# Kernel optimization log

Hardware: AMD Instinct MI355X
Metric: run time of the kernel (lower is better)

## Reference

```python
import jax, jax.numpy as jnp
import numpy as np

B, S, D, H, HD = 4096, 50, 32, 4, 8
SCALE = 1.0 / (8 ** 0.5)


def setup_inputs() -> dict:
    key = jax.random.key(0)
    ks = jax.random.split(key, 12)
    inp = {
        'Q': jax.random.normal(ks[0], (B, S, D), dtype=jnp.float32),
        'K': jax.random.normal(ks[1], (B, S, D), dtype=jnp.float32),
        'V': jax.random.normal(ks[2], (B, S, D), dtype=jnp.float32),
        'mask': jax.random.randint(ks[3], (B, 1, S, S), 0, 2).astype(jnp.bool_),
        # Linear weights (stored as [in, out]; equivalent math to torch's x @ W.T + b)
        'WQ': jax.random.normal(ks[4], (D, D), dtype=jnp.float32) * 0.1,
        'bQ': jnp.zeros((D,), dtype=jnp.float32),
        'WK': jax.random.normal(ks[5], (D, D), dtype=jnp.float32) * 0.1,
        'bK': jnp.zeros((D,), dtype=jnp.float32),
        'WV': jax.random.normal(ks[6], (D, D), dtype=jnp.float32) * 0.1,
        'bV': jnp.zeros((D,), dtype=jnp.float32),
        'WO': jax.random.normal(ks[7], (D, D), dtype=jnp.float32) * 0.1,
        'bO': jnp.zeros((D,), dtype=jnp.float32),
    }
    return inp


def reference(Q, K, V, mask, WQ, bQ, WK, bK, WV, bV, WO, bO):
    qSrc = Q
    # fcQ/fcK/fcV are (faithfully) applied twice, as in the original forward
    q = (Q @ WQ + bQ) @ WQ + bQ
    k = (K @ WK + bK) @ WK + bK
    v = (V @ WV + bV) @ WV + bV
    # split heads: [B, S, D] -> [B, H, S, HD]
    q = q.reshape(B, S, H, HD).transpose(0, 2, 1, 3)
    k = k.reshape(B, S, H, HD).transpose(0, 2, 1, 3)
    v = v.reshape(B, S, H, HD).transpose(0, 2, 1, 3)
    score = jnp.einsum('bhqd,bhkd->bhqk', q, k) * SCALE
    score = jnp.where(mask, -jnp.inf, score)
    attn = jax.nn.softmax(score, axis=-1)
    ctx = jnp.einsum('bhqk,bhkd->bhqd', attn, v)
    ctx = ctx.transpose(0, 2, 1, 3).reshape(B, S, D)
    out = ctx @ WO + bO  # dropout is identity in eval mode
    return qSrc + out
```

## Files before the change

### kernel.cpp

```cpp
#include <hip/hip_runtime.h>

#define NB 4096
constexpr float kQscale = 0.35355339059327378f * 1.4426950408889634f;

constexpr int ST = 40;
constexpr int SP = 72;
constexpr int SV = 72;
constexpr int OFF_W  = 0;
constexpr int OFF_A  = 5120;
constexpr int OFF_C  = 7680;
constexpr int OFF_B  = 10240;
constexpr int OFF_V2 = 12800;
constexpr int SH_LEN = 15104;

typedef __attribute__((ext_vector_type(8))) short bf16x8;
typedef __attribute__((ext_vector_type(4))) float f32x4;

__device__ __forceinline__ unsigned cvt2(float lo, float hi) {
  unsigned u;
  asm("v_cvt_pk_bf16_f32 %0, %1, %2" : "=v"(u) : "v"(lo), "v"(hi));
  return u;
}
__device__ __forceinline__ float fexp2(float x) {
  float r;
  asm("v_exp_f32 %0, %1" : "=v"(r) : "v"(x));
  return r;
}

__global__ __launch_bounds__(256) void mha(
    const float* __restrict__ Qg, const float* __restrict__ Kg,
    const float* __restrict__ Vg, const void* __restrict__ maskg,
    const float* __restrict__ WQg, const float* __restrict__ bQg,
    const float* __restrict__ WKg, const float* __restrict__ bKg,
    const float* __restrict__ WVg, const float* __restrict__ bVg,
    const float* __restrict__ WOg, const float* __restrict__ bOg,
    float* __restrict__ outg)
{
  __shared__ __align__(16) short SH[SH_LEN];
  __shared__ __align__(16) float sBias[128];
  __shared__ unsigned sRaw[80];
  __shared__ unsigned sMask[128];

  const int t = threadIdx.x;
  const int b = blockIdx.x;
  const int lane = t & 63;
  const int wv = t >> 6;
  const int c = lane & 15, g = lane >> 4;
  const int myrow = wv*16 + c;

  auto stage_tile = [&](const float* __restrict__ src, int dstOff) {
    #pragma unroll
    for (int it = 0; it < 2; ++it) {
      const int idx = t + it*256;
      if (idx < 400) {
        const float4 x = ((const float4*)src)[idx];
        const int s = idx >> 3, qd = idx & 7;
        *(uint2*)&SH[dstOff + s*ST + qd*4] = make_uint2(cvt2(x.x, x.y), cvt2(x.z, x.w));
      }
    }
  };

  auto projX = [&](int xOff, int wm, int biasOff, int yOff, float scale) {
    const bf16x8 xb = *(const bf16x8*)&SH[xOff + myrow*ST + g*8];
    #pragma unroll
    for (int Ni = 0; Ni < 2; ++Ni) {
      const bf16x8 wa = *(const bf16x8*)&SH[OFF_W + wm*1280 + (Ni*16 + c)*ST + g*8];
      const float4 bv = *(const float4*)&sBias[biasOff + Ni*16 + g*4];
      f32x4 acc = {bv.x, bv.y, bv.z, bv.w};
      acc = __builtin_amdgcn_mfma_f32_16x16x32_bf16(wa, xb, acc, 0, 0, 0);
      *(uint2*)&SH[yOff + myrow*ST + Ni*16 + g*4] =
          make_uint2(cvt2(acc[0]*scale, acc[1]*scale), cvt2(acc[2]*scale, acc[3]*scale));
    }
  };

  stage_tile(Kg + b*1600, OFF_A);
  stage_tile(Qg + b*1600, OFF_C);
  stage_tile(Vg + b*1600, OFF_B);
  #pragma unroll
  for (int m = 0; m < 4; ++m) {
    const float* Wp = (m == 0) ? WQg : (m == 1) ? WKg : (m == 2) ? WVg : WOg;
    const float4 x = ((const float4*)Wp)[t];
    const int k = t >> 3, d0 = (t & 7)*4;
    const unsigned u0 = cvt2(x.x, x.y), u1 = cvt2(x.z, x.w);
    SH[OFF_W + m*1280 + (d0+0)*ST + k] = (short)(u0 & 0xFFFF);
    SH[OFF_W + m*1280 + (d0+1)*ST + k] = (short)(u0 >> 16);
    SH[OFF_W + m*1280 + (d0+2)*ST + k] = (short)(u1 & 0xFFFF);
    SH[OFF_W + m*1280 + (d0+3)*ST + k] = (short)(u1 >> 16);
  }
  if      (t < 32)  sBias[t] = bQg[t];
  else if (t < 64)  sBias[t] = bKg[t-32];
  else if (t < 96)  sBias[t] = bVg[t-64];
  else if (t < 128) sBias[t] = bOg[t-96];
  {
    const unsigned w64 = ((const unsigned*)maskg)[lane];
    const bool byteMask = (__ballot(w64 > 1u) != 0ull);
    const int mbase = b * 2500;
    for (int ch = wv*10; ch < wv*10 + 10; ++ch) {
      const int idx = ch*64 + lane;
      unsigned val = 0;
      if (idx < 2500) {
        val = byteMask ? (unsigned)((const unsigned char*)maskg)[mbase + idx]
                       : (unsigned)((const unsigned*)maskg)[mbase + idx];
      }
      const unsigned long long m = __ballot(val != 0u);
      if (lane == 0) {
        sRaw[ch*2]     = (unsigned)m;
        sRaw[ch*2 + 1] = (unsigned)(m >> 32);
      }
    }
  }
  __syncthreads();

  if (t < 100) {
    const int i = t >> 1, half = t & 1;
    const int bitpos = 50*i + half*32;
    const int a = bitpos >> 5, sh = bitpos & 31;
    unsigned w = sRaw[a] >> sh;
    if (sh) w |= sRaw[a+1] << (32 - sh);
    sMask[t] = w;
  }
  projX(OFF_A, 1, 32, OFF_A, 1.f);
  projX(OFF_A, 1, 32, OFF_A, 1.f);
  projX(OFF_B, 2, 64, OFF_B, 1.f);
  {
    const bf16x8 a = *(const bf16x8*)&SH[OFF_B + myrow*ST + g*8];
    #pragma unroll
    for (int Nj = 0; Nj < 2; ++Nj) {
      const bf16x8 bb = *(const bf16x8*)&SH[OFF_W + 2*1280 + (Nj*16 + c)*ST + g*8];
      const float bv = sBias[64 + Nj*16 + c];
      f32x4 acc = {bv, bv, bv, bv};
      acc = __builtin_amdgcn_mfma_f32_16x16x32_bf16(a, bb, acc, 0, 0, 0);
      const int j0 = wv*16 + g*4;
      const float v0 = (j0+0 < 50) ? acc[0] : 0.f;
      const float v1 = (j0+1 < 50) ? acc[1] : 0.f;
      const float v2 = (j0+2 < 50) ? acc[2] : 0.f;
      const float v3 = (j0+3 < 50) ? acc[3] : 0.f;
      *(uint2*)&SH[OFF_V2 + (Nj*16 + c)*SV + j0] = make_uint2(cvt2(v0,v1), cvt2(v2,v3));
    }
  }
  projX(OFF_C, 0, 0, OFF_C, 1.f);
  projX(OFF_C, 0, 0, OFF_C, kQscale);
  __syncthreads();

  f32x4 s[4][4];
  {
    const bf16x8 qb = *(const bf16x8*)&SH[OFF_C + myrow*ST + g*8];
    const bf16x8 zf = {0,0,0,0,0,0,0,0};
    #pragma unroll
    for (int Ni = 0; Ni < 4; ++Ni) {
      const bf16x8 kf = *(const bf16x8*)&SH[OFF_A + (Ni*16 + c)*ST + g*8];
      #pragma unroll
      for (int h = 0; h < 4; ++h) {
        const bf16x8 af = (g == h) ? kf : zf;
        f32x4 z = {0.f, 0.f, 0.f, 0.f};
        s[h][Ni] = __builtin_amdgcn_mfma_f32_16x16x32_bf16(af, qb, z, 0, 0, 0);
      }
    }
  }
  __syncthreads();

  const unsigned m0 = (myrow < 50) ? sMask[myrow*2]     : 0xFFFFFFFFu;
  const unsigned m1 = (myrow < 50) ? sMask[myrow*2 + 1] : 0xFFFFFFFFu;
  bool keep[4][4];
  #pragma unroll
  for (int Ni = 0; Ni < 4; ++Ni) {
    const unsigned w = (Ni < 2) ? m0 : m1;
    #pragma unroll
    for (int r = 0; r < 4; ++r) {
      const int key = Ni*16 + g*4 + r;
      keep[Ni][r] = (key < 50) && (((w >> (key & 31)) & 1u) == 0u);
    }
  }

  short* SPp = &SH[OFF_A];
  #pragma unroll
  for (int h = 0; h < 4; ++h) {
    float ps[4][4];
    float rs = 0.f;
    #pragma unroll
    for (int Ni = 0; Ni < 4; ++Ni) {
      #pragma unroll
      for (int r = 0; r < 4; ++r) {
        const float e = fexp2(s[h][Ni][r]);
        const float p = keep[Ni][r] ? e : 0.f;
        ps[Ni][r] = p;
        rs += p;
      }
    }
    rs += __shfl_xor(rs, 16);
    rs += __shfl_xor(rs, 32);
    const float ri = __builtin_amdgcn_rcpf(rs);
    #pragma unroll
    for (int Ni = 0; Ni < 4; ++Ni)
      *(uint2*)&SPp[myrow*SP + Ni*16 + g*4] =
          make_uint2(cvt2(ps[Ni][0], ps[Ni][1]), cvt2(ps[Ni][2], ps[Ni][3]));
    f32x4 cac = {0.f, 0.f, 0.f, 0.f};
    #pragma unroll
    for (int ks = 0; ks < 2; ++ks) {
      const bf16x8 vf = *(const bf16x8*)&SH[OFF_V2 + (h*8 + (c & 7))*SV + ks*32 + g*8];
      const bf16x8 pf = *(const bf16x8*)&SPp[myrow*SP + ks*32 + g*8];
      cac = __builtin_amdgcn_mfma_f32_16x16x32_bf16(vf, pf, cac, 0, 0, 0);
    }
    if (g < 2)
      *(uint2*)&SH[OFF_B + myrow*ST + h*8 + g*4] =
          make_uint2(cvt2(cac[0]*ri, cac[1]*ri), cvt2(cac[2]*ri, cac[3]*ri));
  }

  {
    const bf16x8 af = *(const bf16x8*)&SH[OFF_B + myrow*ST + g*8];
    #pragma unroll
    for (int Nj = 0; Nj < 2; ++Nj) {
      const bf16x8 bbf = *(const bf16x8*)&SH[OFF_W + 3*1280 + (Nj*16 + c)*ST + g*8];
      const float bv = sBias[96 + Nj*16 + c];
      f32x4 o = {bv, bv, bv, bv};
      o = __builtin_amdgcn_mfma_f32_16x16x32_bf16(af, bbf, o, 0, 0, 0);
      #pragma unroll
      for (int r = 0; r < 4; ++r) {
        const int row = wv*16 + g*4 + r;
        if (row < 50) {
          const int gi = b*1600 + row*32 + Nj*16 + c;
          outg[gi] = o[r] + Qg[gi];
        }
      }
    }
  }
}

extern "C" void kernel_launch(void* const* d_in, const int* in_sizes, int n_in,
                              void* d_out, int out_size, void* d_ws, size_t ws_size,
                              hipStream_t stream) {
  const float* Q  = (const float*)d_in[0];
  const float* K  = (const float*)d_in[1];
  const float* V  = (const float*)d_in[2];
  const void*  M  = d_in[3];
  const float* WQ = (const float*)d_in[4];
  const float* bQ = (const float*)d_in[5];
  const float* WK = (const float*)d_in[6];
  const float* bK = (const float*)d_in[7];
  const float* WV = (const float*)d_in[8];
  const float* bV = (const float*)d_in[9];
  const float* WO = (const float*)d_in[10];
  const float* bO = (const float*)d_in[11];
  float* out = (float*)d_out;
  (void)d_ws; (void)ws_size; (void)in_sizes; (void)n_in; (void)out_size;

  hipLaunchKernelGGL(mha, dim3(NB), dim3(256), 0, stream,
                     Q, K, V, M, WQ, bQ, WK, bK, WV, bV, WO, bO, out);
}
```

Measured before the change: 63.78 us.

## Interleave Q/K/V projection passes and compute per-head scores inside softmax loop

```diff
diff --git a/kernel.cpp b/kernel.cpp
--- a/kernel.cpp
+++ b/kernel.cpp
@@ -60,8 +60,7 @@
     }
   };
 
-  auto projX = [&](int xOff, int wm, int biasOff, int yOff, float scale) {
-    const bf16x8 xb = *(const bf16x8*)&SH[xOff + myrow*ST + g*8];
+  auto projStep = [&](bf16x8 xb, int wm, int biasOff, int yOff, float scale) {
     #pragma unroll
     for (int Ni = 0; Ni < 2; ++Ni) {
       const bf16x8 wa = *(const bf16x8*)&SH[OFF_W + wm*1280 + (Ni*16 + c)*ST + g*8];
@@ -95,7 +94,9 @@
     const unsigned w64 = ((const unsigned*)maskg)[lane];
     const bool byteMask = (__ballot(w64 > 1u) != 0ull);
     const int mbase = b * 2500;
-    for (int ch = wv*10; ch < wv*10 + 10; ++ch) {
+    #pragma unroll
+    for (int cc = 0; cc < 10; ++cc) {
+      const int ch = wv*10 + cc;
       const int idx = ch*64 + lane;
       unsigned val = 0;
       if (idx < 2500) {
@@ -119,88 +120,88 @@
     if (sh) w |= sRaw[a+1] << (32 - sh);
     sMask[t] = w;
   }
-  projX(OFF_A, 1, 32, OFF_A, 1.f);
-  projX(OFF_A, 1, 32, OFF_A, 1.f);
-  projX(OFF_B, 2, 64, OFF_B, 1.f);
-  {
-    const bf16x8 a = *(const bf16x8*)&SH[OFF_B + myrow*ST + g*8];
-    #pragma unroll
-    for (int Nj = 0; Nj < 2; ++Nj) {
-      const bf16x8 bb = *(const bf16x8*)&SH[OFF_W + 2*1280 + (Nj*16 + c)*ST + g*8];
-      const float bv = sBias[64 + Nj*16 + c];
-      f32x4 acc = {bv, bv, bv, bv};
-      acc = __builtin_amdgcn_mfma_f32_16x16x32_bf16(a, bb, acc, 0, 0, 0);
-      const int j0 = wv*16 + g*4;
-      const float v0 = (j0+0 < 50) ? acc[0] : 0.f;
-      const float v1 = (j0+1 < 50) ? acc[1] : 0.f;
-      const float v2 = (j0+2 < 50) ? acc[2] : 0.f;
-      const float v3 = (j0+3 < 50) ? acc[3] : 0.f;
-      *(uint2*)&SH[OFF_V2 + (Nj*16 + c)*SV + j0] = make_uint2(cvt2(v0,v1), cvt2(v2,v3));
-    }
-  }
-  projX(OFF_C, 0, 0, OFF_C, 1.f);
-  projX(OFF_C, 0, 0, OFF_C, kQscale);
+  {
+    const bf16x8 aK = *(const bf16x8*)&SH[OFF_A + myrow*ST + g*8];
+    const bf16x8 aV = *(const bf16x8*)&SH[OFF_B + myrow*ST + g*8];
+    const bf16x8 aQ = *(const bf16x8*)&SH[OFF_C + myrow*ST + g*8];
+    projStep(aK, 1, 32, OFF_A, 1.f);
+    projStep(aV, 2, 64, OFF_B, 1.f);
+    projStep(aQ, 0, 0,  OFF_C, 1.f);
+  }
+  {
+    const bf16x8 aK = *(const bf16x8*)&SH[OFF_A + myrow*ST + g*8];
+    const bf16x8 aV = *(const bf16x8*)&SH[OFF_B + myrow*ST + g*8];
+    const bf16x8 aQ = *(const bf16x8*)&SH[OFF_C + myrow*ST + g*8];
+    projStep(aK, 1, 32, OFF_A, 1.f);
+    {
+      #pragma unroll
+      for (int Nj = 0; Nj < 2; ++Nj) {
+        const bf16x8 bb = *(const bf16x8*)&SH[OFF_W + 2*1280 + (Nj*16 + c)*ST + g*8];
+        const float bv = sBias[64 + Nj*16 + c];
+        f32x4 acc = {bv, bv, bv, bv};
+        acc = __builtin_amdgcn_mfma_f32_16x16x32_bf16(aV, bb, acc, 0, 0, 0);
+        const int j0 = wv*16 + g*4;
+        const float v0 = (j0+0 < 50) ? acc[0] : 0.f;
+        const float v1 = (j0+1 < 50) ? acc[1] : 0.f;
+        const float v2 = (j0+2 < 50) ? acc[2] : 0.f;
+        const float v3 = (j0+3 < 50) ? acc[3] : 0.f;
+        *(uint2*)&SH[OFF_V2 + (Nj*16 + c)*SV + j0] = make_uint2(cvt2(v0,v1), cvt2(v2,v3));
+      }
+    }
+    projStep(aQ, 0, 0, OFF_C, kQscale);
+  }
   __syncthreads();
 
-  f32x4 s[4][4];
-  {
-    const bf16x8 qb = *(const bf16x8*)&SH[OFF_C + myrow*ST + g*8];
-    const bf16x8 zf = {0,0,0,0,0,0,0,0};
-    #pragma unroll
-    for (int Ni = 0; Ni < 4; ++Ni) {
-      const bf16x8 kf = *(const bf16x8*)&SH[OFF_A + (Ni*16 + c)*ST + g*8];
-      #pragma unroll
-      for (int h = 0; h < 4; ++h) {
-        const bf16x8 af = (g == h) ? kf : zf;
-        f32x4 z = {0.f, 0.f, 0.f, 0.f};
-        s[h][Ni] = __builtin_amdgcn_mfma_f32_16x16x32_bf16(af, qb, z, 0, 0, 0);
-      }
-    }
-  }
-  __syncthreads();
-
+  const bf16x8 qb = *(const bf16x8*)&SH[OFF_C + myrow*ST + g*8];
+  bf16x8 kf[4];
+  #pragma unroll
+  for (int Ni = 0; Ni < 4; ++Ni)
+    kf[Ni] = *(const bf16x8*)&SH[OFF_A + (Ni*16 + c)*ST + g*8];
   const unsigned m0 = (myrow < 50) ? sMask[myrow*2]     : 0xFFFFFFFFu;
   const unsigned m1 = (myrow < 50) ? sMask[myrow*2 + 1] : 0xFFFFFFFFu;
-  bool keep[4][4];
-  #pragma unroll
-  for (int Ni = 0; Ni < 4; ++Ni) {
-    const unsigned w = (Ni < 2) ? m0 : m1;
-    #pragma unroll
-    for (int r = 0; r < 4; ++r) {
-      const int key = Ni*16 + g*4 + r;
-      keep[Ni][r] = (key < 50) && (((w >> (key & 31)) & 1u) == 0u);
-    }
-  }
+  __syncthreads();
 
   short* SPp = &SH[OFF_A];
+  const bf16x8 zf = {0,0,0,0,0,0,0,0};
   #pragma unroll
   for (int h = 0; h < 4; ++h) {
-    float ps[4][4];
+    const bf16x8 vf0 = *(const bf16x8*)&SH[OFF_V2 + (h*8 + (c & 7))*SV + g*8];
+    const bf16x8 vf1 = *(const bf16x8*)&SH[OFF_V2 + (h*8 + (c & 7))*SV + 32 + g*8];
+    const bf16x8 qh = (g == h) ? qb : zf;
+    f32x4 s[4];
+    #pragma unroll
+    for (int Ni = 0; Ni < 4; ++Ni) {
+      f32x4 z = {0.f, 0.f, 0.f, 0.f};
+      s[Ni] = __builtin_amdgcn_mfma_f32_16x16x32_bf16(kf[Ni], qh, z, 0, 0, 0);
+    }
     float rs = 0.f;
+    unsigned pk[8];
     #pragma unroll
     for (int Ni = 0; Ni < 4; ++Ni) {
+      const unsigned w = (Ni < 2) ? m0 : m1;
+      float p[4];
       #pragma unroll
       for (int r = 0; r < 4; ++r) {
-        const float e = fexp2(s[h][Ni][r]);
-        const float p = keep[Ni][r] ? e : 0.f;
-        ps[Ni][r] = p;
-        rs += p;
-      }
+        const int key = Ni*16 + g*4 + r;
+        const bool keep = (key < 50) && (((w >> (key & 31)) & 1u) == 0u);
+        const float e = fexp2(s[Ni][r]);
+        p[r] = keep ? e : 0.f;
+        rs += p[r];
+      }
+      pk[Ni*2]   = cvt2(p[0], p[1]);
+      pk[Ni*2+1] = cvt2(p[2], p[3]);
     }
     rs += __shfl_xor(rs, 16);
     rs += __shfl_xor(rs, 32);
     const float ri = __builtin_amdgcn_rcpf(rs);
     #pragma unroll
     for (int Ni = 0; Ni < 4; ++Ni)
-      *(uint2*)&SPp[myrow*SP + Ni*16 + g*4] =
-          make_uint2(cvt2(ps[Ni][0], ps[Ni][1]), cvt2(ps[Ni][2], ps[Ni][3]));
+      *(uint2*)&SPp[myrow*SP + Ni*16 + g*4] = make_uint2(pk[Ni*2], pk[Ni*2+1]);
+    const bf16x8 pf0 = *(const bf16x8*)&SPp[myrow*SP + g*8];
+    const bf16x8 pf1 = *(const bf16x8*)&SPp[myrow*SP + 32 + g*8];
     f32x4 cac = {0.f, 0.f, 0.f, 0.f};
-    #pragma unroll
-    for (int ks = 0; ks < 2; ++ks) {
-      const bf16x8 vf = *(const bf16x8*)&SH[OFF_V2 + (h*8 + (c & 7))*SV + ks*32 + g*8];
-      const bf16x8 pf = *(const bf16x8*)&SPp[myrow*SP + ks*32 + g*8];
-      cac = __builtin_amdgcn_mfma_f32_16x16x32_bf16(vf, pf, cac, 0, 0, 0);
-    }
+    cac = __builtin_amdgcn_mfma_f32_16x16x32_bf16(vf0, pf0, cac, 0, 0, 0);
+    cac = __builtin_amdgcn_mfma_f32_16x16x32_bf16(vf1, pf1, cac, 0, 0, 0);
     if (g < 2)
       *(uint2*)&SH[OFF_B + myrow*ST + h*8 + g*4] =
           make_uint2(cvt2(cac[0]*ri, cac[1]*ri), cvt2(cac[2]*ri, cac[3]*ri));
```

Result: faster. 59.86 us (-6.1%).
